# Kernel tuning notes

Hardware: AMD Instinct MI355X
Metric: run time of the kernel (lower is better)

## Reference

```python
import jax, jax.numpy as jnp
import numpy as np

VOCAB = 32000
EMBED = 512
DEP_SIZE = 64
QKV = 512
B, S = 16, 1024
NEG = -1e10


def setup_inputs() -> dict:
    key = jax.random.key(0)
    ks = jax.random.split(key, 16)
    inputs = jax.random.randint(ks[0], (B, S), 0, VOCAB)
    dependency = jax.random.randint(ks[1], (B, S, S), 0, DEP_SIZE)
    embed_table = jax.random.normal(ks[2], (VOCAB, EMBED), dtype=jnp.float32) * 0.02
    dep_table = jax.random.normal(ks[3], (DEP_SIZE, 1), dtype=jnp.float32) * 0.02
    dep_table = dep_table.at[0].set(0.0)  # padding_idx=0
    sc = 1.0 / np.sqrt(EMBED)
    Wq = jax.random.normal(ks[4], (EMBED, QKV), dtype=jnp.float32) * sc
    bq = jnp.zeros((QKV,), jnp.float32)
    Wk = jax.random.normal(ks[5], (EMBED, QKV), dtype=jnp.float32) * sc
    bk = jnp.zeros((QKV,), jnp.float32)
    Wv = jax.random.normal(ks[6], (EMBED, QKV), dtype=jnp.float32) * sc
    bv = jnp.zeros((QKV,), jnp.float32)
    scv = 1.0 / np.sqrt(QKV)
    W1 = jax.random.normal(ks[7], (QKV, QKV), dtype=jnp.float32) * scv
    b1 = jnp.zeros((QKV,), jnp.float32)
    W2 = jax.random.normal(ks[8], (QKV, QKV), dtype=jnp.float32) * scv
    b2 = jnp.zeros((QKV,), jnp.float32)
    return dict(inputs=inputs, dependency=dependency, embed_table=embed_table,
                dep_table=dep_table, Wq=Wq, bq=bq, Wk=Wk, bk=bk, Wv=Wv, bv=bv,
                W1=W1, b1=b1, W2=W2, b2=b2)


def reference(inputs, dependency, embed_table, dep_table, Wq, bq, Wk, bk, Wv, bv, W1, b1, W2, b2):
    x = jnp.take(embed_table, inputs, axis=0)                  # [B,S,E]
    dep_emb = jnp.take(dep_table, dependency, axis=0)[..., 0]  # [B,S,S]
    q = x @ Wq + bq                                            # [B,S,D]
    k = x @ Wk + bk
    v = x @ Wv + bv
    attn = jnp.einsum('bqd,bkd->bqk', q, k) * dep_emb          # [B,S,S]
    attn = jnp.where(dependency == 0, NEG, attn)
    weights = jax.nn.softmax(attn, axis=-1)
    wm = jnp.einsum('bqk,bkd->bqd', weights, v)                # fused weighted sum
    wm = jnp.tanh(wm @ W1 + b1) @ W2 + b2
    return wm, weights
```

## Files before the change

kernel.cpp:

```cpp
#include <hip/hip_runtime.h>

typedef __attribute__((ext_vector_type(8))) short short8;
typedef __attribute__((ext_vector_type(4))) float floatx4;

#define LSTR 40

__device__ __forceinline__ float b2f(unsigned short u) {
  return __uint_as_float(((unsigned int)u) << 16);
}
__device__ __forceinline__ unsigned short f2b(float f) {
  unsigned int u = __float_as_uint(f);
  unsigned int r = (u + 0x7FFFu + ((u >> 16) & 1u)) >> 16;
  return (unsigned short)r;
}
__device__ __forceinline__ uint4 ld8f(const float* p) {
  float4 a = *(const float4*)p;
  float4 b = *(const float4*)(p + 4);
  uint4 r;
  r.x = (unsigned int)f2b(a.x) | ((unsigned int)f2b(a.y) << 16);
  r.y = (unsigned int)f2b(a.z) | ((unsigned int)f2b(a.w) << 16);
  r.z = (unsigned int)f2b(b.x) | ((unsigned int)f2b(b.y) << 16);
  r.w = (unsigned int)f2b(b.z) | ((unsigned int)f2b(b.w) << 16);
  return r;
}

template<int AF32, int CF32, int ACT>
__global__ __launch_bounds__(256, 2) void gemm_bt(
    const void* __restrict__ Av,
    const unsigned short* __restrict__ Bt,
    const float* __restrict__ bias,
    void* __restrict__ Cv,
    const int* __restrict__ arow,
    int M, int N, int K,
    long aBatch, long bBatch, long cBatch)
{
  __shared__ unsigned short ldsA[128 * LSTR];
  __shared__ unsigned short ldsB[128 * LSTR];

  const int b = blockIdx.z;
  const unsigned short* Ab16 = (const unsigned short*)Av + (size_t)b * aBatch;
  const float*          Ab32 = (const float*)Av          + (size_t)b * aBatch;
  const unsigned short* Bb = Bt + (size_t)b * bBatch;

  const int m0 = blockIdx.y * 128, n0 = blockIdx.x * 128;
  const int tid = threadIdx.x;
  const int wave = tid >> 6, lane = tid & 63;
  const int quad = lane >> 4, l16 = lane & 15;
  const int wy = wave >> 1, wx = wave & 1;
  const int r0 = tid >> 2;
  const int s0 = (tid & 3) * 8;

  floatx4 acc[4][4];
#pragma unroll
  for (int i = 0; i < 4; i++)
#pragma unroll
    for (int j = 0; j < 4; j++)
      acc[i][j] = (floatx4){0.f, 0.f, 0.f, 0.f};

  size_t ra0, ra1;
  {
    int gm0 = m0 + r0, gm1 = gm0 + 64;
    ra0 = arow ? (size_t)arow[gm0] : (size_t)gm0;
    ra1 = arow ? (size_t)arow[gm1] : (size_t)gm1;
  }
  const size_t rb0 = (size_t)(n0 + r0), rb1 = rb0 + 64;

  for (int k0 = 0; k0 < K; k0 += 32) {
    uint4 av0, av1;
    if (AF32) {
      av0 = ld8f(Ab32 + ra0 * K + k0 + s0);
      av1 = ld8f(Ab32 + ra1 * K + k0 + s0);
    } else {
      av0 = *(const uint4*)(Ab16 + ra0 * K + k0 + s0);
      av1 = *(const uint4*)(Ab16 + ra1 * K + k0 + s0);
    }
    uint4 bv0 = *(const uint4*)(Bb + rb0 * K + k0 + s0);
    uint4 bv1 = *(const uint4*)(Bb + rb1 * K + k0 + s0);
    __syncthreads();
    *(uint4*)&ldsA[r0 * LSTR + s0] = av0;
    *(uint4*)&ldsA[(r0 + 64) * LSTR + s0] = av1;
    *(uint4*)&ldsB[r0 * LSTR + s0] = bv0;
    *(uint4*)&ldsB[(r0 + 64) * LSTR + s0] = bv1;
    __syncthreads();

    short8 af[4], bfr[4];
#pragma unroll
    for (int i = 0; i < 4; i++)
      af[i] = *(const short8*)&ldsA[(wy * 64 + i * 16 + l16) * LSTR + quad * 8];
#pragma unroll
    for (int j = 0; j < 4; j++)
      bfr[j] = *(const short8*)&ldsB[(wx * 64 + j * 16 + l16) * LSTR + quad * 8];
#pragma unroll
    for (int i = 0; i < 4; i++)
#pragma unroll
      for (int j = 0; j < 4; j++)
        acc[i][j] = __builtin_amdgcn_mfma_f32_16x16x32_bf16(af[i], bfr[j], acc[i][j], 0, 0, 0);
  }

  float bv[4];
#pragma unroll
  for (int j = 0; j < 4; j++) {
    int n = n0 + wx * 64 + j * 16 + l16;
    bv[j] = bias ? bias[n] : 0.f;
  }
  float*          Cf = (float*)Cv          + (size_t)b * cBatch;
  unsigned short* Ch = (unsigned short*)Cv + (size_t)b * cBatch;
#pragma unroll
  for (int i = 0; i < 4; i++) {
#pragma unroll
    for (int r = 0; r < 4; r++) {
      int m = m0 + wy * 64 + i * 16 + quad * 4 + r;
      size_t base = (size_t)m * N + (n0 + wx * 64 + l16);
#pragma unroll
      for (int j = 0; j < 4; j++) {
        float v = acc[i][j][r] + bv[j];
        if (ACT == 1) v = tanhf(v);
        if (CF32) Cf[base + j * 16] = v;
        else      Ch[base + j * 16] = f2b(v);
      }
    }
  }
}

__global__ __launch_bounds__(256, 2) void score_kernel(
    const unsigned short* __restrict__ Q,
    const unsigned short* __restrict__ Kmat,
    const int* __restrict__ dep,
    const float* __restrict__ dep_table,
    float* __restrict__ E)
{
  __shared__ unsigned short ldsA[128 * LSTR];
  __shared__ unsigned short ldsB[128 * LSTR];
  __shared__ float dtab[64];

  const int tid = threadIdx.x;
  if (tid < 64) dtab[tid] = dep_table[tid];

  const int b = blockIdx.z;
  const unsigned short* Ab = Q + (size_t)b * (1024 * 512);
  const unsigned short* Bb = Kmat + (size_t)b * (1024 * 512);

  const int m0 = blockIdx.y * 128, n0 = blockIdx.x * 128;
  const int wave = tid >> 6, lane = tid & 63;
  const int quad = lane >> 4, l16 = lane & 15;
  const int wy = wave >> 1, wx = wave & 1;
  const int r0 = tid >> 2, s0 = (tid & 3) * 8;

  floatx4 acc[4][4];
#pragma unroll
  for (int i = 0; i < 4; i++)
#pragma unroll
    for (int j = 0; j < 4; j++)
      acc[i][j] = (floatx4){0.f, 0.f, 0.f, 0.f};

  for (int k0 = 0; k0 < 512; k0 += 32) {
    uint4 av0 = *(const uint4*)(Ab + (size_t)(m0 + r0) * 512 + k0 + s0);
    uint4 av1 = *(const uint4*)(Ab + (size_t)(m0 + r0 + 64) * 512 + k0 + s0);
    uint4 bv0 = *(const uint4*)(Bb + (size_t)(n0 + r0) * 512 + k0 + s0);
    uint4 bv1 = *(const uint4*)(Bb + (size_t)(n0 + r0 + 64) * 512 + k0 + s0);
    __syncthreads();
    *(uint4*)&ldsA[r0 * LSTR + s0] = av0;
    *(uint4*)&ldsA[(r0 + 64) * LSTR + s0] = av1;
    *(uint4*)&ldsB[r0 * LSTR + s0] = bv0;
    *(uint4*)&ldsB[(r0 + 64) * LSTR + s0] = bv1;
    __syncthreads();

    short8 af[4], bfr[4];
#pragma unroll
    for (int i = 0; i < 4; i++)
      af[i] = *(const short8*)&ldsA[(wy * 64 + i * 16 + l16) * LSTR + quad * 8];
#pragma unroll
    for (int j = 0; j < 4; j++)
      bfr[j] = *(const short8*)&ldsB[(wx * 64 + j * 16 + l16) * LSTR + quad * 8];
#pragma unroll
    for (int i = 0; i < 4; i++)
#pragma unroll
      for (int j = 0; j < 4; j++)
        acc[i][j] = __builtin_amdgcn_mfma_f32_16x16x32_bf16(af[i], bfr[j], acc[i][j], 0, 0, 0);
  }

  const int* depb = dep + (size_t)b * 1024 * 1024;
  float* Eb = E + (size_t)b * 1024 * 1024;
#pragma unroll
  for (int i = 0; i < 4; i++) {
#pragma unroll
    for (int r = 0; r < 4; r++) {
      int m = m0 + wy * 64 + i * 16 + quad * 4 + r;
      const int* drow = depb + (size_t)m * 1024 + (n0 + wx * 64 + l16);
      float* erow = Eb + (size_t)m * 1024 + (n0 + wx * 64 + l16);
#pragma unroll
      for (int j = 0; j < 4; j++) {
        int d = drow[j * 16];
        float s = fminf(fmaxf(acc[i][j][r] * dtab[d & 63], -60.f), 60.f);
        erow[j * 16] = d ? __expf(s) : 0.f;
      }
    }
  }
}

template<int INF32>
__global__ void transpose_to_bf16(const void* __restrict__ in,
                                  unsigned short* __restrict__ out,
                                  int R, int C, long inB, long outB)
{
  __shared__ unsigned short tile[32][33];
  unsigned short* ob = out + (size_t)blockIdx.z * outB;
  int c0 = blockIdx.x * 32, r0 = blockIdx.y * 32;
  int tx = threadIdx.x & 31, ty = threadIdx.x >> 5;
  if (INF32) {
    const float* ib = (const float*)in + (size_t)blockIdx.z * inB;
    for (int i = ty; i < 32; i += 8)
      tile[i][tx] = f2b(ib[(size_t)(r0 + i) * C + (c0 + tx)]);
  } else {
    const unsigned short* ib = (const unsigned short*)in + (size_t)blockIdx.z * inB;
    for (int i = ty; i < 32; i += 8)
      tile[i][tx] = ib[(size_t)(r0 + i) * C + (c0 + tx)];
  }
  __syncthreads();
  for (int i = ty; i < 32; i += 8)
    ob[(size_t)(c0 + i) * R + (r0 + tx)] = tile[tx][i];
}

__global__ void normalize_rows(float* __restrict__ w)
{
  size_t row = blockIdx.x;
  float4* p = (float4*)(w + row * 1024);
  float4 u = p[threadIdx.x];
  float s = (u.x + u.y) + (u.z + u.w);
#pragma unroll
  for (int d = 1; d < 64; d <<= 1) s += __shfl_xor(s, d);
  __shared__ float acc4[4];
  int wave = threadIdx.x >> 6;
  if ((threadIdx.x & 63) == 0) acc4[wave] = s;
  __syncthreads();
  float tot = (acc4[0] + acc4[1]) + (acc4[2] + acc4[3]);
  float inv = tot > 0.f ? 1.f / tot : 0.f;
  u.x *= inv; u.y *= inv; u.z *= inv; u.w *= inv;
  p[threadIdx.x] = u;
}

extern "C" void kernel_launch(void* const* d_in, const int* in_sizes, int n_in,
                              void* d_out, int out_size, void* d_ws, size_t ws_size,
                              hipStream_t stream)
{
  const int*   inputs     = (const int*)d_in[0];
  const int*   dependency = (const int*)d_in[1];
  const float* embed      = (const float*)d_in[2];
  const float* dept       = (const float*)d_in[3];
  const float* Wq = (const float*)d_in[4];   const float* bq = (const float*)d_in[5];
  const float* Wk = (const float*)d_in[6];   const float* bk = (const float*)d_in[7];
  const float* Wv = (const float*)d_in[8];   const float* bvv = (const float*)d_in[9];
  const float* W1 = (const float*)d_in[10];  const float* b1 = (const float*)d_in[11];
  const float* W2 = (const float*)d_in[12];  const float* b2 = (const float*)d_in[13];

  float* out  = (float*)d_out;
  float* wout = out + (size_t)16 * 1024 * 512;

  unsigned short* ws  = (unsigned short*)d_ws;
  unsigned short* q   = ws;
  unsigned short* kx  = ws + 8388608;
  unsigned short* WqT = ws + 16777216;
  unsigned short* WkT = WqT + 262144;
  unsigned short* WvT = WkT + 262144;
  unsigned short* W1T = WvT + 262144;
  unsigned short* W2T = W1T + 262144;
  unsigned short* v   = (unsigned short*)out;
  unsigned short* vT  = q;
  unsigned short* wmp = kx;
  unsigned short* h   = q;

  dim3 blk(256);

  transpose_to_bf16<1><<<dim3(16, 16, 1), blk, 0, stream>>>(Wq, WqT, 512, 512, 0, 0);
  transpose_to_bf16<1><<<dim3(16, 16, 1), blk, 0, stream>>>(Wk, WkT, 512, 512, 0, 0);
  transpose_to_bf16<1><<<dim3(16, 16, 1), blk, 0, stream>>>(Wv, WvT, 512, 512, 0, 0);
  transpose_to_bf16<1><<<dim3(16, 16, 1), blk, 0, stream>>>(W1, W1T, 512, 512, 0, 0);
  transpose_to_bf16<1><<<dim3(16, 16, 1), blk, 0, stream>>>(W2, W2T, 512, 512, 0, 0);

  gemm_bt<1,0,0><<<dim3(4, 128, 1), blk, 0, stream>>>(embed, WqT, bq, q, inputs, 16384, 512, 512, 0, 0, 0);
  gemm_bt<1,0,0><<<dim3(4, 128, 1), blk, 0, stream>>>(embed, WkT, bk, kx, inputs, 16384, 512, 512, 0, 0, 0);
  gemm_bt<1,0,0><<<dim3(4, 128, 1), blk, 0, stream>>>(embed, WvT, bvv, v, inputs, 16384, 512, 512, 0, 0, 0);

  score_kernel<<<dim3(8, 8, 16), blk, 0, stream>>>(q, kx, dependency, dept, wout);

  transpose_to_bf16<0><<<dim3(16, 32, 16), blk, 0, stream>>>(v, vT, 1024, 512, 1024L * 512, 512L * 1024);

  normalize_rows<<<dim3(16384), blk, 0, stream>>>(wout);

  gemm_bt<1,0,0><<<dim3(4, 8, 16), blk, 0, stream>>>(wout, vT, nullptr, wmp, nullptr,
                                                     1024, 512, 1024, 1024L * 1024, 512L * 1024, 1024L * 512);
  gemm_bt<0,0,1><<<dim3(4, 128, 1), blk, 0, stream>>>(wmp, W1T, b1, h, nullptr, 16384, 512, 512, 0, 0, 0);
  gemm_bt<0,1,0><<<dim3(4, 128, 1), blk, 0, stream>>>(h, W2T, b2, out, nullptr, 16384, 512, 512, 0, 0, 0);
}
```

Before: 444.5 us.

## Use direct global-to-LDS loads, fuse QKV GEMMs, stage score epilogue via LDS

Replaces the register-staged GEMM main loop with global_load_lds direct copies into unpadded LDS tiles, shared by every GEMM. The embedding gather runs once into a bf16 buffer, and the three Q/K/V projections become one GEMM over concatenated weights. The five weight transposes merge into one launch. The score epilogue goes through LDS so dependency reads and exp writes are coalesced float4 accesses. Normalize also emits a bf16 copy of the weights so the PV GEMM avoids fp32-to-bf16 conversion, at the cost of unpadded LDS bank conflicts and extra bf16 stores.

```diff
diff --git a/kernel.cpp b/kernel.cpp
--- a/kernel.cpp
+++ b/kernel.cpp
@@ -3,11 +3,6 @@
 typedef __attribute__((ext_vector_type(8))) short short8;
 typedef __attribute__((ext_vector_type(4))) float floatx4;
 
-#define LSTR 40
-
-__device__ __forceinline__ float b2f(unsigned short u) {
-  return __uint_as_float(((unsigned int)u) << 16);
-}
 __device__ __forceinline__ unsigned short f2b(float f) {
   unsigned int u = __float_as_uint(f);
   unsigned int r = (u + 0x7FFFu + ((u >> 16) & 1u)) >> 16;
@@ -24,219 +19,244 @@
   return r;
 }
 
-template<int AF32, int CF32, int ACT>
-__global__ __launch_bounds__(256, 2) void gemm_bt(
-    const void* __restrict__ Av,
-    const unsigned short* __restrict__ Bt,
-    const float* __restrict__ bias,
-    void* __restrict__ Cv,
-    const int* __restrict__ arow,
-    int M, int N, int K,
-    long aBatch, long bBatch, long cBatch)
-{
-  __shared__ unsigned short ldsA[128 * LSTR];
-  __shared__ unsigned short ldsB[128 * LSTR];
-
-  const int b = blockIdx.z;
-  const unsigned short* Ab16 = (const unsigned short*)Av + (size_t)b * aBatch;
-  const float*          Ab32 = (const float*)Av          + (size_t)b * aBatch;
-  const unsigned short* Bb = Bt + (size_t)b * bBatch;
-
+#define GLL(g, l) __builtin_amdgcn_global_load_lds( \
+    (const __attribute__((address_space(1))) unsigned int*)(g), \
+    (__attribute__((address_space(3))) unsigned int*)(l), 16, 0, 0)
+
+__device__ __forceinline__ void kloop(const unsigned short* __restrict__ A,
+                                      const unsigned short* __restrict__ B,
+                                      int K, unsigned short* ldsA, unsigned short* ldsB,
+                                      floatx4 (&acc)[4][4])
+{
+  const int tid = threadIdx.x;
+  const int w = tid >> 6, lane = tid & 63;
+  const int quad = lane >> 4, l16 = lane & 15;
+  const int wy = w >> 1, wx = w & 1;
+  const int rs = 32 * w + (lane >> 2);
+  const int ks = (lane & 3) * 8;
+  const int lo0 = (w * 2) * 512 + lane * 8;
+  const int lo1 = lo0 + 512;
+  const unsigned short* a0 = A + (size_t)rs * K + ks;
+  const unsigned short* a1 = a0 + (size_t)16 * K;
+  const unsigned short* b0 = B + (size_t)rs * K + ks;
+  const unsigned short* b1 = b0 + (size_t)16 * K;
+
+  for (int k0 = 0; k0 < K; k0 += 32) {
+    __syncthreads();
+    GLL(a0 + k0, &ldsA[lo0]);
+    GLL(a1 + k0, &ldsA[lo1]);
+    GLL(b0 + k0, &ldsB[lo0]);
+    GLL(b1 + k0, &ldsB[lo1]);
+    __syncthreads();
+    short8 af[4], bf[4];
+#pragma unroll
+    for (int i = 0; i < 4; i++)
+      af[i] = *(const short8*)&ldsA[(wy * 64 + i * 16 + l16) * 32 + quad * 8];
+#pragma unroll
+    for (int j = 0; j < 4; j++)
+      bf[j] = *(const short8*)&ldsB[(wx * 64 + j * 16 + l16) * 32 + quad * 8];
+#pragma unroll
+    for (int i = 0; i < 4; i++)
+#pragma unroll
+      for (int j = 0; j < 4; j++)
+        acc[i][j] = __builtin_amdgcn_mfma_f32_16x16x32_bf16(af[i], bf[j], acc[i][j], 0, 0, 0);
+  }
+}
+
+__global__ __launch_bounds__(256, 2) void gemm_qkv(
+    const unsigned short* __restrict__ x,
+    const unsigned short* __restrict__ WT,
+    const float* __restrict__ bq, const float* __restrict__ bk, const float* __restrict__ bv,
+    unsigned short* __restrict__ q, unsigned short* __restrict__ kx, unsigned short* __restrict__ v)
+{
+  __shared__ unsigned short ldsA[4096], ldsB[4096];
   const int m0 = blockIdx.y * 128, n0 = blockIdx.x * 128;
-  const int tid = threadIdx.x;
-  const int wave = tid >> 6, lane = tid & 63;
-  const int quad = lane >> 4, l16 = lane & 15;
-  const int wy = wave >> 1, wx = wave & 1;
-  const int r0 = tid >> 2;
-  const int s0 = (tid & 3) * 8;
-
   floatx4 acc[4][4];
 #pragma unroll
   for (int i = 0; i < 4; i++)
 #pragma unroll
-    for (int j = 0; j < 4; j++)
-      acc[i][j] = (floatx4){0.f, 0.f, 0.f, 0.f};
-
-  size_t ra0, ra1;
-  {
-    int gm0 = m0 + r0, gm1 = gm0 + 64;
-    ra0 = arow ? (size_t)arow[gm0] : (size_t)gm0;
-    ra1 = arow ? (size_t)arow[gm1] : (size_t)gm1;
-  }
-  const size_t rb0 = (size_t)(n0 + r0), rb1 = rb0 + 64;
-
-  for (int k0 = 0; k0 < K; k0 += 32) {
-    uint4 av0, av1;
-    if (AF32) {
-      av0 = ld8f(Ab32 + ra0 * K + k0 + s0);
-      av1 = ld8f(Ab32 + ra1 * K + k0 + s0);
-    } else {
-      av0 = *(const uint4*)(Ab16 + ra0 * K + k0 + s0);
-      av1 = *(const uint4*)(Ab16 + ra1 * K + k0 + s0);
-    }
-    uint4 bv0 = *(const uint4*)(Bb + rb0 * K + k0 + s0);
-    uint4 bv1 = *(const uint4*)(Bb + rb1 * K + k0 + s0);
-    __syncthreads();
-    *(uint4*)&ldsA[r0 * LSTR + s0] = av0;
-    *(uint4*)&ldsA[(r0 + 64) * LSTR + s0] = av1;
-    *(uint4*)&ldsB[r0 * LSTR + s0] = bv0;
-    *(uint4*)&ldsB[(r0 + 64) * LSTR + s0] = bv1;
-    __syncthreads();
-
-    short8 af[4], bfr[4];
-#pragma unroll
-    for (int i = 0; i < 4; i++)
-      af[i] = *(const short8*)&ldsA[(wy * 64 + i * 16 + l16) * LSTR + quad * 8];
-#pragma unroll
-    for (int j = 0; j < 4; j++)
-      bfr[j] = *(const short8*)&ldsB[(wx * 64 + j * 16 + l16) * LSTR + quad * 8];
-#pragma unroll
-    for (int i = 0; i < 4; i++)
-#pragma unroll
-      for (int j = 0; j < 4; j++)
-        acc[i][j] = __builtin_amdgcn_mfma_f32_16x16x32_bf16(af[i], bfr[j], acc[i][j], 0, 0, 0);
-  }
-
-  float bv[4];
-#pragma unroll
-  for (int j = 0; j < 4; j++) {
-    int n = n0 + wx * 64 + j * 16 + l16;
-    bv[j] = bias ? bias[n] : 0.f;
-  }
-  float*          Cf = (float*)Cv          + (size_t)b * cBatch;
-  unsigned short* Ch = (unsigned short*)Cv + (size_t)b * cBatch;
-#pragma unroll
-  for (int i = 0; i < 4; i++) {
+    for (int j = 0; j < 4; j++) acc[i][j] = (floatx4){0.f, 0.f, 0.f, 0.f};
+
+  kloop(x + (size_t)m0 * 512, WT + (size_t)n0 * 512, 512, ldsA, ldsB, acc);
+
+  const int seg = n0 >> 9, nloc = n0 & 511;
+  unsigned short* C = seg == 0 ? q : (seg == 1 ? kx : v);
+  const float* bias = seg == 0 ? bq : (seg == 1 ? bk : bv);
+  const int lane = threadIdx.x & 63, w = threadIdx.x >> 6;
+  const int quad = lane >> 4, l16 = lane & 15, wy = w >> 1, wx = w & 1;
+  float bvv[4];
+#pragma unroll
+  for (int j = 0; j < 4; j++) bvv[j] = bias[nloc + wx * 64 + j * 16 + l16];
+#pragma unroll
+  for (int i = 0; i < 4; i++)
 #pragma unroll
     for (int r = 0; r < 4; r++) {
       int m = m0 + wy * 64 + i * 16 + quad * 4 + r;
-      size_t base = (size_t)m * N + (n0 + wx * 64 + l16);
+      unsigned short* crow = C + (size_t)m * 512 + nloc + wx * 64 + l16;
+#pragma unroll
+      for (int j = 0; j < 4; j++) crow[j * 16] = f2b(acc[i][j][r] + bvv[j]);
+    }
+}
+
+template<int CF32, int ACT>
+__global__ __launch_bounds__(256, 2) void gemm2(
+    const unsigned short* __restrict__ A, const unsigned short* __restrict__ Bt,
+    const float* __restrict__ bias, void* __restrict__ Cv,
+    int N, int K, long aB, long bB, long cB)
+{
+  __shared__ unsigned short ldsA[4096], ldsB[4096];
+  const int b = blockIdx.z;
+  const int m0 = blockIdx.y * 128, n0 = blockIdx.x * 128;
+  floatx4 acc[4][4];
+#pragma unroll
+  for (int i = 0; i < 4; i++)
+#pragma unroll
+    for (int j = 0; j < 4; j++) acc[i][j] = (floatx4){0.f, 0.f, 0.f, 0.f};
+
+  kloop(A + (size_t)b * aB + (size_t)m0 * K, Bt + (size_t)b * bB + (size_t)n0 * K,
+        K, ldsA, ldsB, acc);
+
+  const int lane = threadIdx.x & 63, w = threadIdx.x >> 6;
+  const int quad = lane >> 4, l16 = lane & 15, wy = w >> 1, wx = w & 1;
+  float bvv[4];
+#pragma unroll
+  for (int j = 0; j < 4; j++)
+    bvv[j] = bias ? bias[n0 + wx * 64 + j * 16 + l16] : 0.f;
+  float*          Cf = (float*)Cv          + (size_t)b * cB;
+  unsigned short* Ch = (unsigned short*)Cv + (size_t)b * cB;
+#pragma unroll
+  for (int i = 0; i < 4; i++)
+#pragma unroll
+    for (int r = 0; r < 4; r++) {
+      int m = m0 + wy * 64 + i * 16 + quad * 4 + r;
+      size_t base = (size_t)m * N + n0 + wx * 64 + l16;
 #pragma unroll
       for (int j = 0; j < 4; j++) {
-        float v = acc[i][j][r] + bv[j];
-        if (ACT == 1) v = tanhf(v);
-        if (CF32) Cf[base + j * 16] = v;
-        else      Ch[base + j * 16] = f2b(v);
+        float vv = acc[i][j][r] + bvv[j];
+        if (ACT == 1) vv = tanhf(vv);
+        if (CF32) Cf[base + j * 16] = vv;
+        else      Ch[base + j * 16] = f2b(vv);
       }
     }
-  }
-}
-
+}
+
+#define CST 132
 __global__ __launch_bounds__(256, 2) void score_kernel(
-    const unsigned short* __restrict__ Q,
-    const unsigned short* __restrict__ Kmat,
-    const int* __restrict__ dep,
-    const float* __restrict__ dep_table,
+    const unsigned short* __restrict__ Q, const unsigned short* __restrict__ Km,
+    const int* __restrict__ dep, const float* __restrict__ dept,
     float* __restrict__ E)
 {
-  __shared__ unsigned short ldsA[128 * LSTR];
-  __shared__ unsigned short ldsB[128 * LSTR];
+  __shared__ union {
+    struct { unsigned short a[4096]; unsigned short b[4096]; } s;
+    float c[32 * CST];
+  } sm;
   __shared__ float dtab[64];
-
   const int tid = threadIdx.x;
-  if (tid < 64) dtab[tid] = dep_table[tid];
+  if (tid < 64) dtab[tid] = dept[tid];
 
   const int b = blockIdx.z;
-  const unsigned short* Ab = Q + (size_t)b * (1024 * 512);
-  const unsigned short* Bb = Kmat + (size_t)b * (1024 * 512);
-
   const int m0 = blockIdx.y * 128, n0 = blockIdx.x * 128;
-  const int wave = tid >> 6, lane = tid & 63;
-  const int quad = lane >> 4, l16 = lane & 15;
-  const int wy = wave >> 1, wx = wave & 1;
-  const int r0 = tid >> 2, s0 = (tid & 3) * 8;
-
   floatx4 acc[4][4];
 #pragma unroll
   for (int i = 0; i < 4; i++)
 #pragma unroll
-    for (int j = 0; j < 4; j++)
-      acc[i][j] = (floatx4){0.f, 0.f, 0.f, 0.f};
-
-  for (int k0 = 0; k0 < 512; k0 += 32) {
-    uint4 av0 = *(const uint4*)(Ab + (size_t)(m0 + r0) * 512 + k0 + s0);
-    uint4 av1 = *(const uint4*)(Ab + (size_t)(m0 + r0 + 64) * 512 + k0 + s0);
-    uint4 bv0 = *(const uint4*)(Bb + (size_t)(n0 + r0) * 512 + k0 + s0);
-    uint4 bv1 = *(const uint4*)(Bb + (size_t)(n0 + r0 + 64) * 512 + k0 + s0);
-    __syncthreads();
-    *(uint4*)&ldsA[r0 * LSTR + s0] = av0;
-    *(uint4*)&ldsA[(r0 + 64) * LSTR + s0] = av1;
-    *(uint4*)&ldsB[r0 * LSTR + s0] = bv0;
-    *(uint4*)&ldsB[(r0 + 64) * LSTR + s0] = bv1;
-    __syncthreads();
-
-    short8 af[4], bfr[4];
-#pragma unroll
-    for (int i = 0; i < 4; i++)
-      af[i] = *(const short8*)&ldsA[(wy * 64 + i * 16 + l16) * LSTR + quad * 8];
-#pragma unroll
-    for (int j = 0; j < 4; j++)
-      bfr[j] = *(const short8*)&ldsB[(wx * 64 + j * 16 + l16) * LSTR + quad * 8];
-#pragma unroll
-    for (int i = 0; i < 4; i++)
-#pragma unroll
-      for (int j = 0; j < 4; j++)
-        acc[i][j] = __builtin_amdgcn_mfma_f32_16x16x32_bf16(af[i], bfr[j], acc[i][j], 0, 0, 0);
-  }
-
+    for (int j = 0; j < 4; j++) acc[i][j] = (floatx4){0.f, 0.f, 0.f, 0.f};
+
+  kloop(Q + (size_t)b * (1024 * 512) + (size_t)m0 * 512,
+        Km + (size_t)b * (1024 * 512) + (size_t)n0 * 512,
+        512, sm.s.a, sm.s.b, acc);
+
+  const int lane = tid & 63, w = tid >> 6;
+  const int quad = lane >> 4, l16 = lane & 15, wy = w >> 1, wx = w & 1;
   const int* depb = dep + (size_t)b * 1024 * 1024;
   float* Eb = E + (size_t)b * 1024 * 1024;
+  const int cr = tid >> 3, cb = (tid & 7) * 16;
+
 #pragma unroll
   for (int i = 0; i < 4; i++) {
-#pragma unroll
-    for (int r = 0; r < 4; r++) {
-      int m = m0 + wy * 64 + i * 16 + quad * 4 + r;
-      const int* drow = depb + (size_t)m * 1024 + (n0 + wx * 64 + l16);
-      float* erow = Eb + (size_t)m * 1024 + (n0 + wx * 64 + l16);
-#pragma unroll
-      for (int j = 0; j < 4; j++) {
-        int d = drow[j * 16];
-        float s = fminf(fmaxf(acc[i][j][r] * dtab[d & 63], -60.f), 60.f);
-        erow[j * 16] = d ? __expf(s) : 0.f;
-      }
+    __syncthreads();
+#pragma unroll
+    for (int j = 0; j < 4; j++)
+#pragma unroll
+      for (int r = 0; r < 4; r++)
+        sm.c[(wy * 16 + quad * 4 + r) * CST + wx * 64 + j * 16 + l16] = acc[i][j][r];
+    __syncthreads();
+    const int m = m0 + (cr >> 4) * 64 + i * 16 + (cr & 15);
+    const int* dr = depb + (size_t)m * 1024 + n0 + cb;
+    float* er = Eb + (size_t)m * 1024 + n0 + cb;
+    const float* crow = &sm.c[cr * CST + cb];
+#pragma unroll
+    for (int c = 0; c < 4; c++) {
+      int4 d = *(const int4*)(dr + c * 4);
+      float4 s = *(const float4*)(crow + c * 4);
+      float4 e;
+      e.x = d.x ? __expf(fminf(fmaxf(s.x * dtab[d.x & 63], -60.f), 60.f)) : 0.f;
+      e.y = d.y ? __expf(fminf(fmaxf(s.y * dtab[d.y & 63], -60.f), 60.f)) : 0.f;
+      e.z = d.z ? __expf(fminf(fmaxf(s.z * dtab[d.z & 63], -60.f), 60.f)) : 0.f;
+      e.w = d.w ? __expf(fminf(fmaxf(s.w * dtab[d.w & 63], -60.f), 60.f)) : 0.f;
+      *(float4*)(er + c * 4) = e;
     }
   }
 }
 
-template<int INF32>
-__global__ void transpose_to_bf16(const void* __restrict__ in,
-                                  unsigned short* __restrict__ out,
-                                  int R, int C, long inB, long outB)
+__global__ void build_x(const float* __restrict__ embed, const int* __restrict__ inputs,
+                        unsigned short* __restrict__ x)
+{
+  const int row = blockIdx.x * 4 + (threadIdx.x >> 6);
+  const int lane = threadIdx.x & 63;
+  const float* src = embed + (size_t)inputs[row] * 512 + lane * 8;
+  *(uint4*)&x[(size_t)row * 512 + lane * 8] = ld8f(src);
+}
+
+__global__ void trans_w(const float* s0, const float* s1, const float* s2,
+                        const float* s3, const float* s4, unsigned short* dst)
 {
   __shared__ unsigned short tile[32][33];
-  unsigned short* ob = out + (size_t)blockIdx.z * outB;
+  const int z = blockIdx.z;
+  const float* src = z == 0 ? s0 : z == 1 ? s1 : z == 2 ? s2 : z == 3 ? s3 : s4;
+  unsigned short* ob = dst + (size_t)z * 262144;
   int c0 = blockIdx.x * 32, r0 = blockIdx.y * 32;
   int tx = threadIdx.x & 31, ty = threadIdx.x >> 5;
-  if (INF32) {
-    const float* ib = (const float*)in + (size_t)blockIdx.z * inB;
-    for (int i = ty; i < 32; i += 8)
-      tile[i][tx] = f2b(ib[(size_t)(r0 + i) * C + (c0 + tx)]);
-  } else {
-    const unsigned short* ib = (const unsigned short*)in + (size_t)blockIdx.z * inB;
-    for (int i = ty; i < 32; i += 8)
-      tile[i][tx] = ib[(size_t)(r0 + i) * C + (c0 + tx)];
-  }
+  for (int i = ty; i < 32; i += 8)
+    tile[i][tx] = f2b(src[(size_t)(r0 + i) * 512 + (c0 + tx)]);
   __syncthreads();
   for (int i = ty; i < 32; i += 8)
-    ob[(size_t)(c0 + i) * R + (r0 + tx)] = tile[tx][i];
-}
-
-__global__ void normalize_rows(float* __restrict__ w)
+    ob[(size_t)(c0 + i) * 512 + (r0 + tx)] = tile[tx][i];
+}
+
+__global__ void trans_v(const unsigned short* __restrict__ in, unsigned short* __restrict__ out)
+{
+  __shared__ unsigned short tile[32][33];
+  const unsigned short* ib = in + (size_t)blockIdx.z * (1024 * 512);
+  unsigned short* ob = out + (size_t)blockIdx.z * (512 * 1024);
+  int c0 = blockIdx.x * 32, r0 = blockIdx.y * 32;
+  int tx = threadIdx.x & 31, ty = threadIdx.x >> 5;
+  for (int i = ty; i < 32; i += 8)
+    tile[i][tx] = ib[(size_t)(r0 + i) * 512 + (c0 + tx)];
+  __syncthreads();
+  for (int i = ty; i < 32; i += 8)
+    ob[(size_t)(c0 + i) * 1024 + (r0 + tx)] = tile[tx][i];
+}
+
+__global__ void normalize_rows(float* __restrict__ wf, unsigned short* __restrict__ wb)
 {
   size_t row = blockIdx.x;
-  float4* p = (float4*)(w + row * 1024);
+  float4* p = (float4*)(wf + row * 1024);
   float4 u = p[threadIdx.x];
   float s = (u.x + u.y) + (u.z + u.w);
 #pragma unroll
   for (int d = 1; d < 64; d <<= 1) s += __shfl_xor(s, d);
   __shared__ float acc4[4];
-  int wave = threadIdx.x >> 6;
-  if ((threadIdx.x & 63) == 0) acc4[wave] = s;
+  if ((threadIdx.x & 63) == 0) acc4[threadIdx.x >> 6] = s;
   __syncthreads();
   float tot = (acc4[0] + acc4[1]) + (acc4[2] + acc4[3]);
   float inv = tot > 0.f ? 1.f / tot : 0.f;
   u.x *= inv; u.y *= inv; u.z *= inv; u.w *= inv;
   p[threadIdx.x] = u;
+  uint2 pk;
+  pk.x = (unsigned int)f2b(u.x) | ((unsigned int)f2b(u.y) << 16);
+  pk.y = (unsigned int)f2b(u.z) | ((unsigned int)f2b(u.w) << 16);
+  *(uint2*)&wb[row * 1024 + threadIdx.x * 4] = pk;
 }
 
 extern "C" void kernel_launch(void* const* d_in, const int* in_sizes, int n_in,
@@ -254,41 +274,37 @@
   const float* W2 = (const float*)d_in[12];  const float* b2 = (const float*)d_in[13];
 
   float* out  = (float*)d_out;
-  float* wout = out + (size_t)16 * 1024 * 512;
-
-  unsigned short* ws  = (unsigned short*)d_ws;
-  unsigned short* q   = ws;
-  unsigned short* kx  = ws + 8388608;
-  unsigned short* WqT = ws + 16777216;
-  unsigned short* WkT = WqT + 262144;
-  unsigned short* WvT = WkT + 262144;
-  unsigned short* W1T = WvT + 262144;
-  unsigned short* W2T = W1T + 262144;
-  unsigned short* v   = (unsigned short*)out;
-  unsigned short* vT  = q;
-  unsigned short* wmp = kx;
-  unsigned short* h   = q;
+  float* wout = out + (size_t)8388608;
+
+  unsigned short* ws   = (unsigned short*)d_ws;
+  unsigned short* q    = ws;
+  unsigned short* kx   = ws + 8388608;
+  unsigned short* WTc  = ws + 16777216;
+  unsigned short* W1T  = ws + 17563648;
+  unsigned short* W2T  = ws + 17825792;
+  unsigned short* wbf  = ws;
+  unsigned short* h    = ws;
+
+  unsigned short* x    = (unsigned short*)wout;
+  unsigned short* v    = (unsigned short*)out;
+  unsigned short* vT   = (unsigned short*)out + 8388608;
+  unsigned short* wmp  = (unsigned short*)out;
 
   dim3 blk(256);
 
-  transpose_to_bf16<1><<<dim3(16, 16, 1), blk, 0, stream>>>(Wq, WqT, 512, 512, 0, 0);
-  transpose_to_bf16<1><<<dim3(16, 16, 1), blk, 0, stream>>>(Wk, WkT, 512, 512, 0, 0);
-  transpose_to_bf16<1><<<dim3(16, 16, 1), blk, 0, stream>>>(Wv, WvT, 512, 512, 0, 0);
-  transpose_to_bf16<1><<<dim3(16, 16, 1), blk, 0, stream>>>(W1, W1T, 512, 512, 0, 0);
-  transpose_to_bf16<1><<<dim3(16, 16, 1), blk, 0, stream>>>(W2, W2T, 512, 512, 0, 0);
-
-  gemm_bt<1,0,0><<<dim3(4, 128, 1), blk, 0, stream>>>(embed, WqT, bq, q, inputs, 16384, 512, 512, 0, 0, 0);
-  gemm_bt<1,0,0><<<dim3(4, 128, 1), blk, 0, stream>>>(embed, WkT, bk, kx, inputs, 16384, 512, 512, 0, 0, 0);
-  gemm_bt<1,0,0><<<dim3(4, 128, 1), blk, 0, stream>>>(embed, WvT, bvv, v, inputs, 16384, 512, 512, 0, 0, 0);
+  trans_w<<<dim3(16, 16, 5), blk, 0, stream>>>(Wq, Wk, Wv, W1, W2, WTc);
+  build_x<<<dim3(4096), blk, 0, stream>>>(embed, inputs, x);
+
+  gemm_qkv<<<dim3(12, 128, 1), blk, 0, stream>>>(x, WTc, bq, bk, bvv, q, kx, v);
 
   score_kernel<<<dim3(8, 8, 16), blk, 0, stream>>>(q, kx, dependency, dept, wout);
 
-  transpose_to_bf16<0><<<dim3(16, 32, 16), blk, 0, stream>>>(v, vT, 1024, 512, 1024L * 512, 512L * 1024);
-
-  normalize_rows<<<dim3(16384), blk, 0, stream>>>(wout);
-
-  gemm_bt<1,0,0><<<dim3(4, 8, 16), blk, 0, stream>>>(wout, vT, nullptr, wmp, nullptr,
-                                                     1024, 512, 1024, 1024L * 1024, 512L * 1024, 1024L * 512);
-  gemm_bt<0,0,1><<<dim3(4, 128, 1), blk, 0, stream>>>(wmp, W1T, b1, h, nullptr, 16384, 512, 512, 0, 0, 0);
-  gemm_bt<0,1,0><<<dim3(4, 128, 1), blk, 0, stream>>>(h, W2T, b2, out, nullptr, 16384, 512, 512, 0, 0, 0);
-}
+  trans_v<<<dim3(16, 32, 16), blk, 0, stream>>>(v, vT);
+
+  normalize_rows<<<dim3(16384), blk, 0, stream>>>(wout, wbf);
+
+  gemm2<0, 0><<<dim3(4, 8, 16), blk, 0, stream>>>(wbf, vT, nullptr, wmp,
+                                                  512, 1024, 1024L * 1024, 512L * 1024, 1024L * 512);
+  gemm2<0, 1><<<dim3(4, 128, 1), blk, 0, stream>>>(wmp, W1T, b1, h, 512, 512, 0, 0, 0);
+  gemm2<1, 0><<<dim3(4, 128, 1), blk, 0, stream>>>(h, W2T, b2, out, 512, 512, 0, 0, 0);
+}
```

Result: faster. 405.0 us (-8.9%).
